# Kernel tuning notes

Measured on AMD Instinct MI355X. Metric: run time of the kernel, lower is better.

## Reference

```python
import jax, jax.numpy as jnp
import numpy as np

N = 100000   # nodes
E = 1600000  # edges (avg degree 16)
DIM = 3      # coordinate dims
R = 3        # pseudo-coordinate dim
C = 32       # channels / Gaussian kernels
F = 64       # non-coordinate node features


def setup_inputs() -> dict:
    key = jax.random.key(0)
    k1, k2, k3, k4, k5 = jax.random.split(key, 5)
    features = jax.random.normal(k1, (N, DIM + F), dtype=jnp.float32)
    edge_index = jax.random.randint(k2, (E, 2), 0, N, dtype=jnp.int32)  # (row=i, col=j) per edge
    w_dense = jax.random.normal(k3, (DIM, R), dtype=jnp.float32) / jnp.sqrt(jnp.float32(DIM))  # lecun-ish
    b_dense = jnp.zeros((R,), dtype=jnp.float32)
    mu = jax.random.normal(k4, (C, N, R), dtype=jnp.float32) * 0.1
    # sigma initialized positive (abs of lecun normal in the original); keep bounded away from 0
    sig = jax.random.uniform(k5, (C, N, R), dtype=jnp.float32, minval=0.1, maxval=1.0)
    return {"features": features, "edge_index": edge_index,
            "w_dense": w_dense, "b_dense": b_dense, "mu": mu, "sig": sig}


def reference(features, edge_index, w_dense, b_dense, mu, sig):
    coords = features[:, :DIM]          # [N, 3]
    h = features[:, DIM:]               # [N, F]
    src = edge_index[:, 0]              # row index i per edge
    dst = edge_index[:, 1]              # col index j per edge
    # per-edge pseudo-coordinates: tanh(Dense_r(x_j - x_i))
    u = jnp.tanh((coords[dst] - coords[src]) @ w_dense + b_dense)      # [E, R]
    # Gaussian-mixture edge weight per (channel, edge), mu/sigma gathered at row node i
    diff = u[None, :, :] - mu[:, src, :]                               # [C, E, R]
    w = jnp.exp(-0.5 * jnp.sum(diff * diff / sig[:, src, :], axis=-1)) # [C, E]
    # (A o W) @ H summed over feature axis == sum_j w[c,i,j] * sum_f H[j,f]
    msg = w * jnp.sum(h, axis=-1)[dst][None, :]                        # [C, E]
    agg = jax.ops.segment_sum(msg.T, src, num_segments=N)              # [N, C]
    return jnp.concatenate([coords, agg], axis=-1)                     # [N, DIM + C]
```

## Files before the change

### kernel.cpp

```cpp
#include <hip/hip_runtime.h>

#define DIMV 3
#define RV 3
#define CV 32
#define FV 64
#define ROWF 67
#define ROWO 35
#define CAP 48
#define SCAN_T 1024
#define NGRP 8
#define BSH 6
#define BNODES 64
#define SEGCAP 256

__device__ __forceinline__ float fast_tanh(float x) {
    float ex = __expf(2.0f * x);
    return (ex - 1.0f) * __builtin_amdgcn_rcpf(ex + 1.0f);
}

__global__ void prep_kernel(const float* __restrict__ features,
                            float4* __restrict__ nd,
                            int* __restrict__ counts,
                            int* __restrict__ bcur, int nbc,
                            float* __restrict__ out, int N) {
    int gid = blockIdx.x * blockDim.x + threadIdx.x;
    if (gid < N) counts[gid] = 0;
    if (gid < nbc) bcur[gid] = 0;
    int node = gid >> 6;
    int lane = threadIdx.x & 63;
    if (node >= N) return;
    const float* row = features + (size_t)node * ROWF;
    float f0 = row[lane];
    float f1 = (lane < ROWF - 64) ? row[64 + lane] : 0.0f;
    float v = (lane >= DIMV ? f0 : 0.0f) + f1;
    for (int off = 32; off > 0; off >>= 1) v += __shfl_xor(v, off, 64);
    float c0 = __shfl(f0, 0, 64);
    float c1 = __shfl(f0, 1, 64);
    float c2 = __shfl(f0, 2, 64);
    if (lane == 0) nd[node] = make_float4(c0, c1, c2, v);
    if (lane < DIMV) out[(size_t)node * ROWO + lane] = f0;
}

__global__ void bin_kernel(const int2* __restrict__ ei2,
                           int* __restrict__ bcur,
                           unsigned int* __restrict__ bins, int E, int NB) {
    int grp = blockIdx.x & (NGRP - 1);
    int stride = gridDim.x * blockDim.x;
    for (int e = blockIdx.x * blockDim.x + threadIdx.x; e < E; e += stride) {
        unsigned long long v =
            __builtin_nontemporal_load((const unsigned long long*)ei2 + e);
        int s = (int)(v & 0xffffffffull);
        int d = (int)(v >> 32);
        int b = s >> BSH;
        int slot = atomicAdd(bcur + grp * NB + b, 1);
        if (slot < SEGCAP)
            bins[(size_t)(grp * NB + b) * SEGCAP + slot] =
                ((unsigned)(s & (BNODES - 1)) << 17) | (unsigned)d;
    }
}

__global__ void bucket_scatter_kernel(const int* __restrict__ bcur,
                                      const unsigned int* __restrict__ bins,
                                      const float4* __restrict__ nd,
                                      const float* __restrict__ wd,
                                      const float* __restrict__ bd,
                                      int* __restrict__ counts,
                                      float4* __restrict__ ue_pad, int N, int NB) {
    __shared__ float4 ue_lds[BNODES * CAP];
    __shared__ float4 snd[BNODES];
    __shared__ int lcnt[BNODES];
    int b = blockIdx.x;
    int base = b << BSH;
    int nn = N - base; if (nn > BNODES) nn = BNODES;
    int t = threadIdx.x;
    if (t < BNODES) {
        lcnt[t] = 0;
        snd[t] = (t < nn) ? nd[base + t] : make_float4(0.f, 0.f, 0.f, 0.f);
    }
    __syncthreads();
    float w0 = wd[0], w1 = wd[1], w2 = wd[2];
    float w3 = wd[3], w4 = wd[4], w5 = wd[5];
    float w6 = wd[6], w7 = wd[7], w8 = wd[8];
    float b0 = bd[0], b1 = bd[1], b2 = bd[2];
    for (int g = 0; g < NGRP; ++g) {
        int cnt = bcur[g * NB + b];
        if (cnt > SEGCAP) cnt = SEGCAP;
        const unsigned int* seg = bins + (size_t)(g * NB + b) * SEGCAP;
        for (int i = t; i < cnt; i += blockDim.x) {
            unsigned p = seg[i];
            int sl = p >> 17;
            int d  = p & 0x1FFFF;
            float4 pd = nd[d];
            int k = atomicAdd(&lcnt[sl], 1);
            if (k >= CAP) k = CAP - 1;
            float4 ps = snd[sl];
            float dx = pd.x - ps.x, dy = pd.y - ps.y, dz = pd.z - ps.z;
            float u0 = fast_tanh(dx * w0 + dy * w3 + dz * w6 + b0);
            float u1 = fast_tanh(dx * w1 + dy * w4 + dz * w7 + b1);
            float u2 = fast_tanh(dx * w2 + dy * w5 + dz * w8 + b2);
            ue_lds[sl * CAP + k] = make_float4(u0, u1, u2, pd.w);
        }
    }
    __syncthreads();
    int lane = t & 63;
    int w = t >> 6;
    for (int n = w; n < nn; n += 4) {
        int c = lcnt[n]; if (c > CAP) c = CAP;
        if (lane < c)
            ue_pad[(size_t)(base + n) * CAP + lane] = ue_lds[n * CAP + lane];
    }
    if (t < nn) counts[base + t] = min(lcnt[t], CAP);
}

__global__ void node_pad_kernel(const int* __restrict__ counts,
                                const float4* __restrict__ ue_pad,
                                const float* __restrict__ mu,
                                const float* __restrict__ sig,
                                float* __restrict__ out, int N) {
    __shared__ float4 sm[4][CAP];
    int node = (blockIdx.x * blockDim.x + threadIdx.x) >> 6;
    int lane = threadIdx.x & 63;
    int w = threadIdx.x >> 6;
    int c = lane & 31;
    int half = lane >> 5;
    bool valid = node < N;
    float m0 = 0, m1 = 0, m2 = 0, i0 = 1, i1 = 1, i2 = 1;
    int cnt = 0;
    if (valid) {
        size_t slab = (size_t)N * RV;
        const float* mp = mu + (size_t)c * slab + (size_t)node * RV;
        const float* sp = sig + (size_t)c * slab + (size_t)node * RV;
        m0 = mp[0]; m1 = mp[1]; m2 = mp[2];
        i0 = __builtin_amdgcn_rcpf(sp[0]);
        i1 = __builtin_amdgcn_rcpf(sp[1]);
        i2 = __builtin_amdgcn_rcpf(sp[2]);
        cnt = counts[node];
        if (cnt > CAP) cnt = CAP;
        if (lane < cnt) sm[w][lane] = ue_pad[(size_t)node * CAP + lane];
    }
    __syncthreads();
    float acc = 0.0f;
    for (int k = half; k < cnt; k += 2) {
        float4 q = sm[w][k];
        float d0 = q.x - m0, d1 = q.y - m1, d2 = q.z - m2;
        float t = d0 * d0 * i0 + d1 * d1 * i1 + d2 * d2 * i2;
        acc += __expf(-0.5f * t) * q.w;
    }
    acc += __shfl_xor(acc, 32, 64);
    if (valid && half == 0) out[(size_t)node * ROWO + DIMV + c] = acc;
}


__global__ void hist_kernel(const int2* __restrict__ ei2, int* __restrict__ counts, int E) {
    int e = blockIdx.x * blockDim.x + threadIdx.x;
    if (e >= E) return;
    atomicAdd(counts + ei2[e].x, 1);
}

__global__ void scan_a_kernel(const int* __restrict__ counts, int* __restrict__ offsets,
                              int* __restrict__ partials, int N) {
    __shared__ int sm[SCAN_T];
    int t = threadIdx.x;
    int i = blockIdx.x * SCAN_T + t;
    int c = (i < N) ? counts[i] : 0;
    sm[t] = c;
    __syncthreads();
    for (int off = 1; off < SCAN_T; off <<= 1) {
        int v = (t >= off) ? sm[t - off] : 0;
        __syncthreads();
        sm[t] += v;
        __syncthreads();
    }
    if (i < N) offsets[i] = sm[t] - c;
    if (t == SCAN_T - 1) partials[blockIdx.x] = sm[t];
}

__global__ void scan_b_kernel(int* __restrict__ partials, int B) {
    __shared__ int sm[SCAN_T];
    int t = threadIdx.x;
    int c = (t < B) ? partials[t] : 0;
    sm[t] = c;
    __syncthreads();
    for (int off = 1; off < SCAN_T; off <<= 1) {
        int v = (t >= off) ? sm[t - off] : 0;
        __syncthreads();
        sm[t] += v;
        __syncthreads();
    }
    if (t < B) partials[t] = sm[t] - c;
}

__global__ void scan_c_kernel(int* __restrict__ offsets, const int* __restrict__ partials,
                              int* __restrict__ cursor, int N, int E) {
    int i = blockIdx.x * blockDim.x + threadIdx.x;
    if (i == 0) offsets[N] = E;
    if (i >= N) return;
    int off = offsets[i] + partials[i / SCAN_T];
    offsets[i] = off;
    cursor[i] = off;
}

__global__ void scatter_u_kernel(const int2* __restrict__ ei2, int* __restrict__ cursor,
                                 const float4* __restrict__ nd,
                                 const float* __restrict__ wd, const float* __restrict__ bd,
                                 float4* __restrict__ ue, int E) {
    int e = blockIdx.x * blockDim.x + threadIdx.x;
    if (e >= E) return;
    int2 sd = ei2[e];
    int pos = atomicAdd(cursor + sd.x, 1);
    float4 ps = nd[sd.x];
    float4 pd = nd[sd.y];
    float dx = pd.x - ps.x, dy = pd.y - ps.y, dz = pd.z - ps.z;
    float u0 = fast_tanh(dx * wd[0] + dy * wd[3] + dz * wd[6] + bd[0]);
    float u1 = fast_tanh(dx * wd[1] + dy * wd[4] + dz * wd[7] + bd[1]);
    float u2 = fast_tanh(dx * wd[2] + dy * wd[5] + dz * wd[8] + bd[2]);
    ue[pos] = make_float4(u0, u1, u2, pd.w);
}

__global__ void node_acc2_kernel(const int* __restrict__ offsets,
                                 const float4* __restrict__ ue,
                                 const float* __restrict__ mu,
                                 const float* __restrict__ sig,
                                 float* __restrict__ out, int N) {
    int node = (blockIdx.x * blockDim.x + threadIdx.x) >> 6;
    if (node >= N) return;
    int lane = threadIdx.x & 63;
    int c = lane & 31;
    int half = lane >> 5;
    size_t slab = (size_t)N * RV;
    const float* mp = mu + (size_t)c * slab + (size_t)node * RV;
    const float* sp = sig + (size_t)c * slab + (size_t)node * RV;
    float m0 = mp[0], m1 = mp[1], m2 = mp[2];
    float i0 = __builtin_amdgcn_rcpf(sp[0]);
    float i1 = __builtin_amdgcn_rcpf(sp[1]);
    float i2 = __builtin_amdgcn_rcpf(sp[2]);
    int off0 = offsets[node], off1 = offsets[node + 1];
    float acc = 0.0f;
    for (int i = off0 + half; i < off1; i += 2) {
        float4 q = ue[i];
        float d0 = q.x - m0, d1 = q.y - m1, d2 = q.z - m2;
        float t = d0 * d0 * i0 + d1 * d1 * i1 + d2 * d2 * i2;
        acc += __expf(-0.5f * t) * q.w;
    }
    acc += __shfl_xor(acc, 32, 64);
    if (half == 0) out[(size_t)node * ROWO + DIMV + c] = acc;
}


__global__ void fb_pre_kernel(const float* __restrict__ features,
                              float4* __restrict__ nd, float* __restrict__ out, int N) {
    int gid = blockIdx.x * blockDim.x + threadIdx.x;
    int node = gid >> 6;
    int lane = threadIdx.x & 63;
    if (node >= N) return;
    const float* row = features + (size_t)node * ROWF;
    float f0 = row[lane];
    float f1 = (lane < ROWF - 64) ? row[64 + lane] : 0.0f;
    float v = (lane >= DIMV ? f0 : 0.0f) + f1;
    for (int off = 32; off > 0; off >>= 1) v += __shfl_xor(v, off, 64);
    float c0 = __shfl(f0, 0, 64);
    float c1 = __shfl(f0, 1, 64);
    float c2 = __shfl(f0, 2, 64);
    if (lane == 0) nd[node] = make_float4(c0, c1, c2, v);
    float* orow = out + (size_t)node * ROWO;
    if (lane < DIMV) orow[lane] = f0;
    else if (lane < ROWO) orow[lane] = 0.0f;
}

__global__ void fb_edge_kernel(const int* __restrict__ ei, const float4* __restrict__ nd,
                               const float* __restrict__ wd, const float* __restrict__ bd,
                               const float* __restrict__ mu, const float* __restrict__ sig,
                               float* __restrict__ out, int N, int E) {
    int e = blockIdx.x * blockDim.x + threadIdx.x;
    if (e >= E) return;
    int s = ei[2 * e];
    int d = ei[2 * e + 1];
    float4 ps = nd[s];
    float4 pd = nd[d];
    float dx = pd.x - ps.x, dy = pd.y - ps.y, dz = pd.z - ps.z;
    float u0 = fast_tanh(dx * wd[0] + dy * wd[3] + dz * wd[6] + bd[0]);
    float u1 = fast_tanh(dx * wd[1] + dy * wd[4] + dz * wd[7] + bd[1]);
    float u2 = fast_tanh(dx * wd[2] + dy * wd[5] + dz * wd[8] + bd[2]);
    float hs = pd.w;
    float* oagg = out + (size_t)s * ROWO + DIMV;
    size_t nodeoff = (size_t)s * RV;
    size_t slab = (size_t)N * RV;
#pragma unroll 4
    for (int c = 0; c < CV; ++c) {
        const float* mp = mu + (size_t)c * slab + nodeoff;
        const float* sp = sig + (size_t)c * slab + nodeoff;
        float d0 = u0 - mp[0], d1 = u1 - mp[1], d2 = u2 - mp[2];
        float t = d0 * d0 * __builtin_amdgcn_rcpf(sp[0])
                + d1 * d1 * __builtin_amdgcn_rcpf(sp[1])
                + d2 * d2 * __builtin_amdgcn_rcpf(sp[2]);
        atomicAdd(oagg + c, __expf(-0.5f * t) * hs);
    }
}

extern "C" void kernel_launch(void* const* d_in, const int* in_sizes, int n_in,
                              void* d_out, int out_size, void* d_ws, size_t ws_size,
                              hipStream_t stream) {
    const float* features = (const float*)d_in[0];
    const int*   ei       = (const int*)d_in[1];
    const int2*  ei2      = (const int2*)d_in[1];
    const float* wd       = (const float*)d_in[2];
    const float* bd       = (const float*)d_in[3];
    const float* mu       = (const float*)d_in[4];
    const float* sig      = (const float*)d_in[5];
    float* out = (float*)d_out;

    int N = in_sizes[0] / ROWF;
    int E = in_sizes[1] / 2;
    int B = (N + SCAN_T - 1) / SCAN_T;
    int NB = (N + BNODES - 1) / BNODES;

    size_t cur = 0;
    auto take = [&](size_t bytes) { size_t p = cur; cur += (bytes + 255) & ~(size_t)255; return p; };
    size_t o_nd      = take((size_t)N * sizeof(float4));
    size_t o_counts  = take((size_t)N * sizeof(int));
    size_t o_offsets = take((size_t)(N + 1) * sizeof(int));
    size_t o_cursor  = take((size_t)N * sizeof(int));
    size_t o_part    = take((size_t)SCAN_T * sizeof(int));
    size_t o_bcur    = take((size_t)NGRP * NB * sizeof(int));
    size_t o_bins    = take((size_t)NGRP * NB * SEGCAP * sizeof(unsigned int));
    size_t o_tail    = cur;
    size_t need_pad  = o_tail + (((size_t)N * CAP * sizeof(float4) + 255) & ~(size_t)255);
    size_t need_full = o_tail + (((size_t)E * sizeof(float4) + 255) & ~(size_t)255);

    char* ws = (char*)d_ws;
    float4* nd   = (float4*)(ws + o_nd);
    int* counts  = (int*)(ws + o_counts);
    int* offsets = (int*)(ws + o_offsets);
    int* cursor  = (int*)(ws + o_cursor);
    int* part    = (int*)(ws + o_part);
    int* bcur    = (int*)(ws + o_bcur);
    unsigned int* bins = (unsigned int*)(ws + o_bins);

    if (ws_size >= need_pad && N < (1 << 17)) {
        float4* ue_pad = (float4*)(ws + o_tail);
        prep_kernel<<<(N + 3) / 4, 256, 0, stream>>>(features, nd, counts, bcur, NGRP * NB, out, N);
        bin_kernel<<<2048, 256, 0, stream>>>(ei2, bcur, bins, E, NB);
        bucket_scatter_kernel<<<NB, 256, 0, stream>>>(bcur, bins, nd, wd, bd, counts, ue_pad, N, NB);
        node_pad_kernel<<<(N + 3) / 4, 256, 0, stream>>>(counts, ue_pad, mu, sig, out, N);
    } else if (ws_size >= need_full && B <= SCAN_T) {
        float4* ue = (float4*)(ws + o_tail);
        prep_kernel<<<(N + 3) / 4, 256, 0, stream>>>(features, nd, counts, bcur, 0, out, N);
        hist_kernel<<<(E + 255) / 256, 256, 0, stream>>>(ei2, counts, E);
        scan_a_kernel<<<B, SCAN_T, 0, stream>>>(counts, offsets, part, N);
        scan_b_kernel<<<1, SCAN_T, 0, stream>>>(part, B);
        scan_c_kernel<<<(N + 255) / 256, 256, 0, stream>>>(offsets, part, cursor, N, E);
        scatter_u_kernel<<<(E + 255) / 256, 256, 0, stream>>>(ei2, cursor, nd, wd, bd, ue, E);
        node_acc2_kernel<<<(N + 3) / 4, 256, 0, stream>>>(offsets, ue, mu, sig, out, N);
    } else {
        fb_pre_kernel<<<(N + 3) / 4, 256, 0, stream>>>(features, nd, out, N);
        fb_edge_kernel<<<(E + 255) / 256, 256, 0, stream>>>(ei, nd, wd, bd, mu, sig, out, N, E);
    }
}
```

Before: 293.1 us.

## Fuse bucket scatter with per-node Gaussian accumulation and bin edges by XCC

```diff
diff --git a/kernel.cpp b/kernel.cpp
--- a/kernel.cpp
+++ b/kernel.cpp
@@ -3,19 +3,27 @@
 #define DIMV 3
 #define RV 3
 #define CV 32
-#define FV 64
 #define ROWF 67
 #define ROWO 35
 #define CAP 48
+#define PADSTR 49
 #define SCAN_T 1024
 #define NGRP 8
 #define BSH 6
 #define BNODES 64
-#define SEGCAP 256
+#define SEGCAP 512
+#define CCH 8
+#define MSPAD 193
 
 __device__ __forceinline__ float fast_tanh(float x) {
     float ex = __expf(2.0f * x);
     return (ex - 1.0f) * __builtin_amdgcn_rcpf(ex + 1.0f);
+}
+
+__device__ __forceinline__ int xcc_id() {
+    int x;
+    asm("s_getreg_b32 %0, hwreg(HW_REG_XCC_ID)" : "=s"(x));
+    return x & (NGRP - 1);
 }
 
 __global__ void prep_kernel(const float* __restrict__ features,
@@ -44,7 +52,7 @@
 __global__ void bin_kernel(const int2* __restrict__ ei2,
                            int* __restrict__ bcur,
                            unsigned int* __restrict__ bins, int E, int NB) {
-    int grp = blockIdx.x & (NGRP - 1);
+    int grp = xcc_id();
     int stride = gridDim.x * blockDim.x;
     for (int e = blockIdx.x * blockDim.x + threadIdx.x; e < E; e += stride) {
         unsigned long long v =
@@ -52,23 +60,34 @@
         int s = (int)(v & 0xffffffffull);
         int d = (int)(v >> 32);
         int b = s >> BSH;
-        int slot = atomicAdd(bcur + grp * NB + b, 1);
+        int g = grp;
+        int slot = atomicAdd(bcur + g * NB + b, 1);
+#pragma unroll 1
+        for (int tries = 0; slot >= SEGCAP && tries < NGRP; ++tries) {
+            g = (g + 1) & (NGRP - 1);
+            slot = atomicAdd(bcur + g * NB + b, 1);
+        }
         if (slot < SEGCAP)
-            bins[(size_t)(grp * NB + b) * SEGCAP + slot] =
+            bins[(size_t)(g * NB + b) * SEGCAP + slot] =
                 ((unsigned)(s & (BNODES - 1)) << 17) | (unsigned)d;
     }
 }
 
-__global__ void bucket_scatter_kernel(const int* __restrict__ bcur,
-                                      const unsigned int* __restrict__ bins,
-                                      const float4* __restrict__ nd,
-                                      const float* __restrict__ wd,
-                                      const float* __restrict__ bd,
-                                      int* __restrict__ counts,
-                                      float4* __restrict__ ue_pad, int N, int NB) {
-    __shared__ float4 ue_lds[BNODES * CAP];
+__global__ __launch_bounds__(256, 2)
+void fused_bucket_kernel(const int* __restrict__ bcur,
+                         const unsigned int* __restrict__ bins,
+                         const float4* __restrict__ nd,
+                         const float* __restrict__ wd,
+                         const float* __restrict__ bd,
+                         const float* __restrict__ mu,
+                         const float* __restrict__ sig,
+                         float* __restrict__ out, int N, int NB) {
+    __shared__ float4 ue[BNODES * PADSTR];
     __shared__ float4 snd[BNODES];
     __shared__ int lcnt[BNODES];
+    __shared__ int soff[NGRP + 1];
+    __shared__ float msm[CCH * MSPAD];
+    __shared__ float mss[CCH * MSPAD];
     int b = blockIdx.x;
     int base = b << BSH;
     int nn = N - base; if (nn > BNODES) nn = BNODES;
@@ -77,77 +96,81 @@
         lcnt[t] = 0;
         snd[t] = (t < nn) ? nd[base + t] : make_float4(0.f, 0.f, 0.f, 0.f);
     }
+    if (t < NGRP) {
+        int c = bcur[t * NB + b];
+        soff[t + 1] = (c > SEGCAP) ? SEGCAP : c;
+    }
+    if (t == 0) soff[0] = 0;
+    __syncthreads();
+    if (t == 0) {
+#pragma unroll
+        for (int g = 0; g < NGRP; ++g) soff[g + 1] += soff[g];
+    }
     __syncthreads();
     float w0 = wd[0], w1 = wd[1], w2 = wd[2];
     float w3 = wd[3], w4 = wd[4], w5 = wd[5];
     float w6 = wd[6], w7 = wd[7], w8 = wd[8];
     float b0 = bd[0], b1 = bd[1], b2 = bd[2];
-    for (int g = 0; g < NGRP; ++g) {
-        int cnt = bcur[g * NB + b];
-        if (cnt > SEGCAP) cnt = SEGCAP;
-        const unsigned int* seg = bins + (size_t)(g * NB + b) * SEGCAP;
-        for (int i = t; i < cnt; i += blockDim.x) {
-            unsigned p = seg[i];
-            int sl = p >> 17;
-            int d  = p & 0x1FFFF;
-            float4 pd = nd[d];
-            int k = atomicAdd(&lcnt[sl], 1);
-            if (k >= CAP) k = CAP - 1;
-            float4 ps = snd[sl];
-            float dx = pd.x - ps.x, dy = pd.y - ps.y, dz = pd.z - ps.z;
-            float u0 = fast_tanh(dx * w0 + dy * w3 + dz * w6 + b0);
-            float u1 = fast_tanh(dx * w1 + dy * w4 + dz * w7 + b1);
-            float u2 = fast_tanh(dx * w2 + dy * w5 + dz * w8 + b2);
-            ue_lds[sl * CAP + k] = make_float4(u0, u1, u2, pd.w);
+    int total = soff[NGRP];
+    for (int r = t; r < total; r += 256) {
+        int g = 0;
+#pragma unroll
+        for (int gg = 1; gg < NGRP; ++gg) if (r >= soff[gg]) g = gg;
+        int i = r - soff[g];
+        unsigned p = bins[(size_t)(g * NB + b) * SEGCAP + i];
+        int sl = p >> 17;
+        int d  = p & 0x1FFFF;
+        float4 pd = nd[d];
+        int k = atomicAdd(&lcnt[sl], 1);
+        if (k >= CAP) k = CAP - 1;
+        float4 ps = snd[sl];
+        float dx = pd.x - ps.x, dy = pd.y - ps.y, dz = pd.z - ps.z;
+        float u0 = fast_tanh(dx * w0 + dy * w3 + dz * w6 + b0);
+        float u1 = fast_tanh(dx * w1 + dy * w4 + dz * w7 + b1);
+        float u2 = fast_tanh(dx * w2 + dy * w5 + dz * w8 + b2);
+        ue[sl * PADSTR + k] = make_float4(u0, u1, u2, pd.w);
+    }
+    __syncthreads();
+    int c8 = t & (CCH - 1);
+    int nl = t >> 3;
+    size_t slab = (size_t)N * RV;
+    for (int cc = 0; cc < CV / CCH; ++cc) {
+        for (int f = t; f < CCH * RV * BNODES; f += 256) {
+            int ci = f / (RV * BNODES);
+            int j  = f - ci * (RV * BNODES);
+            float vm = 0.0f, vs = 1.0f;
+            if (j < nn * RV) {
+                size_t gidx = (size_t)(cc * CCH + ci) * slab + (size_t)base * RV + j;
+                vm = mu[gidx];
+                vs = sig[gidx];
+            }
+            msm[ci * MSPAD + j] = vm;
+            mss[ci * MSPAD + j] = vs;
         }
-    }
-    __syncthreads();
-    int lane = t & 63;
-    int w = t >> 6;
-    for (int n = w; n < nn; n += 4) {
-        int c = lcnt[n]; if (c > CAP) c = CAP;
-        if (lane < c)
-            ue_pad[(size_t)(base + n) * CAP + lane] = ue_lds[n * CAP + lane];
-    }
-    if (t < nn) counts[base + t] = min(lcnt[t], CAP);
-}
-
-__global__ void node_pad_kernel(const int* __restrict__ counts,
-                                const float4* __restrict__ ue_pad,
-                                const float* __restrict__ mu,
-                                const float* __restrict__ sig,
-                                float* __restrict__ out, int N) {
-    __shared__ float4 sm[4][CAP];
-    int node = (blockIdx.x * blockDim.x + threadIdx.x) >> 6;
-    int lane = threadIdx.x & 63;
-    int w = threadIdx.x >> 6;
-    int c = lane & 31;
-    int half = lane >> 5;
-    bool valid = node < N;
-    float m0 = 0, m1 = 0, m2 = 0, i0 = 1, i1 = 1, i2 = 1;
-    int cnt = 0;
-    if (valid) {
-        size_t slab = (size_t)N * RV;
-        const float* mp = mu + (size_t)c * slab + (size_t)node * RV;
-        const float* sp = sig + (size_t)c * slab + (size_t)node * RV;
-        m0 = mp[0]; m1 = mp[1]; m2 = mp[2];
-        i0 = __builtin_amdgcn_rcpf(sp[0]);
-        i1 = __builtin_amdgcn_rcpf(sp[1]);
-        i2 = __builtin_amdgcn_rcpf(sp[2]);
-        cnt = counts[node];
-        if (cnt > CAP) cnt = CAP;
-        if (lane < cnt) sm[w][lane] = ue_pad[(size_t)node * CAP + lane];
-    }
-    __syncthreads();
-    float acc = 0.0f;
-    for (int k = half; k < cnt; k += 2) {
-        float4 q = sm[w][k];
-        float d0 = q.x - m0, d1 = q.y - m1, d2 = q.z - m2;
-        float t = d0 * d0 * i0 + d1 * d1 * i1 + d2 * d2 * i2;
-        acc += __expf(-0.5f * t) * q.w;
-    }
-    acc += __shfl_xor(acc, 32, 64);
-    if (valid && half == 0) out[(size_t)node * ROWO + DIMV + c] = acc;
+        __syncthreads();
+#pragma unroll
+        for (int rep = 0; rep < 2; ++rep) {
+            int n = nl + rep * 32;
+            if (n < nn) {
+                int cnt = lcnt[n]; if (cnt > CAP) cnt = CAP;
+                const float* mrow = &msm[c8 * MSPAD + n * RV];
+                const float* srow = &mss[c8 * MSPAD + n * RV];
+                float m0 = mrow[0], m1 = mrow[1], m2 = mrow[2];
+                float i0 = __builtin_amdgcn_rcpf(srow[0]);
+                float i1 = __builtin_amdgcn_rcpf(srow[1]);
+                float i2 = __builtin_amdgcn_rcpf(srow[2]);
+                float acc = 0.0f;
+                for (int k = 0; k < cnt; ++k) {
+                    float4 q = ue[n * PADSTR + k];
+                    float d0 = q.x - m0, d1 = q.y - m1, d2 = q.z - m2;
+                    float t2 = d0 * d0 * i0 + d1 * d1 * i1 + d2 * d2 * i2;
+                    acc += __expf(-0.5f * t2) * q.w;
+                }
+                out[(size_t)(base + n) * ROWO + DIMV + cc * CCH + c8] = acc;
+            }
+        }
+        __syncthreads();
+    }
 }
 
 
@@ -324,8 +347,8 @@
     size_t o_bcur    = take((size_t)NGRP * NB * sizeof(int));
     size_t o_bins    = take((size_t)NGRP * NB * SEGCAP * sizeof(unsigned int));
     size_t o_tail    = cur;
-    size_t need_pad  = o_tail + (((size_t)N * CAP * sizeof(float4) + 255) & ~(size_t)255);
-    size_t need_full = o_tail + (((size_t)E * sizeof(float4) + 255) & ~(size_t)255);
+    size_t need_fused = o_tail;
+    size_t need_full  = o_tail + (((size_t)E * sizeof(float4) + 255) & ~(size_t)255);
 
     char* ws = (char*)d_ws;
     float4* nd   = (float4*)(ws + o_nd);
@@ -336,12 +359,10 @@
     int* bcur    = (int*)(ws + o_bcur);
     unsigned int* bins = (unsigned int*)(ws + o_bins);
 
-    if (ws_size >= need_pad && N < (1 << 17)) {
-        float4* ue_pad = (float4*)(ws + o_tail);
+    if (ws_size >= need_fused && N < (1 << 17)) {
         prep_kernel<<<(N + 3) / 4, 256, 0, stream>>>(features, nd, counts, bcur, NGRP * NB, out, N);
         bin_kernel<<<2048, 256, 0, stream>>>(ei2, bcur, bins, E, NB);
-        bucket_scatter_kernel<<<NB, 256, 0, stream>>>(bcur, bins, nd, wd, bd, counts, ue_pad, N, NB);
-        node_pad_kernel<<<(N + 3) / 4, 256, 0, stream>>>(counts, ue_pad, mu, sig, out, N);
+        fused_bucket_kernel<<<NB, 256, 0, stream>>>(bcur, bins, nd, wd, bd, mu, sig, out, N, NB);
     } else if (ws_size >= need_full && B <= SCAN_T) {
         float4* ue = (float4*)(ws + o_tail);
         prep_kernel<<<(N + 3) / 4, 256, 0, stream>>>(features, nd, counts, bcur, 0, out, N);
```

New measurement: 328.0 us. 11.9% more time.
